# Optimization experiments

Measured on AMD Instinct MI355X. Metric: run time of the kernel, lower is better.

## Reference

```python
import jax, jax.numpy as jnp
import numpy as np
from jax import lax

K = 9  # 3x3 kernel points


def _gather(feat, iy, ix):
    """feat: [B,C,H,W]; iy,ix: [B,K,H,W] int32. Zero padding outside bounds.
    Returns [B,C,K,H,W]."""
    B, C, H, W = feat.shape
    valid = ((iy >= 0) & (iy < H) & (ix >= 0) & (ix < W))
    iyc = jnp.clip(iy, 0, H - 1)
    ixc = jnp.clip(ix, 0, W - 1)
    flat = (iyc * W + ixc).reshape(B, 1, -1)            # [B,1,K*H*W]
    g = jnp.take_along_axis(feat.reshape(B, C, H * W), flat, axis=2)
    g = g.reshape(B, C, K, H, W)
    return g * valid[:, None].astype(feat.dtype)


def _bilinear(feat, ys, xs):
    """feat: [B,C,H,W]; ys,xs: [B,K,H,W] float sampling coords -> [B,C,K,H,W]."""
    y0 = jnp.floor(ys)
    x0 = jnp.floor(xs)
    wy = (ys - y0)[:, None]
    wx = (xs - x0)[:, None]
    y0i = y0.astype(jnp.int32)
    x0i = x0.astype(jnp.int32)
    y1i = y0i + 1
    x1i = x0i + 1
    v00 = _gather(feat, y0i, x0i)
    v01 = _gather(feat, y0i, x1i)
    v10 = _gather(feat, y1i, x0i)
    v11 = _gather(feat, y1i, x1i)
    return (v00 * (1 - wy) * (1 - wx) + v01 * (1 - wy) * wx
            + v10 * wy * (1 - wx) + v11 * wy * wx)


def _deform_layer(x, w_off, b_off, w, b, dilation=1):
    """Modulated deformable 3x3 conv, stride 1, padding=dilation (same size)."""
    B, C, H, W = x.shape
    # offset/mask conv (regular 3x3 conv, same padding)
    om = lax.conv_general_dilated(
        x, w_off, window_strides=(1, 1),
        padding=[(dilation, dilation), (dilation, dilation)],
        rhs_dilation=(dilation, dilation),
        dimension_numbers=('NCHW', 'OIHW', 'NCHW')) + b_off[None, :, None, None]
    off = om[:, :2 * K].reshape(B, K, 2, H, W)   # (dy, dx) per kernel point
    mask = jax.nn.sigmoid(om[:, 2 * K:])         # [B,K,H,W]
    dy = off[:, :, 0]
    dx = off[:, :, 1]
    # base kernel grid offsets (-d, 0, +d)
    ky, kx = jnp.meshgrid(jnp.arange(3), jnp.arange(3), indexing='ij')
    base_y = ((ky.reshape(-1) - 1) * dilation).astype(x.dtype)   # [K]
    base_x = ((kx.reshape(-1) - 1) * dilation).astype(x.dtype)
    gy = jnp.arange(H, dtype=x.dtype)
    gx = jnp.arange(W, dtype=x.dtype)
    ys = gy[None, None, :, None] + base_y[None, :, None, None] + dy  # [B,K,H,W]
    xs = gx[None, None, None, :] + base_x[None, :, None, None] + dx
    sampled = _bilinear(x, ys, xs) * mask[:, None]   # [B,C,K,H,W]
    wk = w.reshape(w.shape[0], w.shape[1], K)        # [O,I,K]
    out = jnp.einsum('bikhw,oik->bohw', sampled, wk) + b[None, :, None, None]
    return out


def setup_inputs() -> dict:
    key = jax.random.key(0)
    ks = jax.random.split(key, 16)
    B, C, H, W = 4, 256, 64, 64
    O = 256
    inp = {'x': jax.random.normal(ks[0], (B, C, H, W), jnp.float32)}
    chans = [(C, C), (C, O), (O, O)]  # layer i==num_layers-2 maps in->out
    for i, (ci, co) in enumerate(chans):
        k = jax.random.split(ks[i + 1], 4)
        # offset conv: 27 = 3*K channels (18 offsets + 9 masks); small init
        inp[f'w_off{i}'] = jax.random.normal(k[0], (3 * K, ci, 3, 3), jnp.float32) * 0.01
        inp[f'b_off{i}'] = jnp.zeros((3 * K,), jnp.float32)
        # deform conv weight: kaiming normal, fan_in = ci*K
        std = np.sqrt(2.0 / (ci * K)).astype(np.float32)
        inp[f'w{i}'] = jax.random.normal(k[1], (co, ci, 3, 3), jnp.float32) * std
        inp[f'b{i}'] = jnp.zeros((co,), jnp.float32)
    return inp


def reference(x, w_off0, b_off0, w0, b0, w_off1, b_off1, w1, b1,
              w_off2, b_off2, w2, b2):
    params = [(w_off0, b_off0, w0, b0),
              (w_off1, b_off1, w1, b1),
              (w_off2, b_off2, w2, b2)]
    for (wo, bo, w, b) in params:
        x = jax.nn.relu(_deform_layer(x, wo, bo, w, b, dilation=1))
    return x
```

## Files before the change

kernel.cpp:

```cpp
#include <hip/hip_runtime.h>
#include <math.h>

#define Bn 4
#define Cn 256
#define Hn 64
#define Wn 64
#define On 256
#define HWn 4096
#define Pn 16384
#define Kc 2304

#define LGKM0 0xc07f

typedef _Float16 half8 __attribute__((ext_vector_type(8)));
typedef float floatx4 __attribute__((ext_vector_type(4)));

__global__ void k_transpose_f2h(const float* __restrict__ in, _Float16* __restrict__ out,
                                int R, int Cc) {
  __shared__ float tile[32][33];
  int b = blockIdx.z;
  int c0 = blockIdx.x * 32, r0 = blockIdx.y * 32;
  const float* ib = in + (size_t)b * R * Cc;
  _Float16* ob = out + (size_t)b * R * Cc;
  int tx = threadIdx.x, ty = threadIdx.y;
#pragma unroll
  for (int i = 0; i < 32; i += 8)
    tile[ty + i][tx] = ib[(size_t)(r0 + ty + i) * Cc + (c0 + tx)];
  __syncthreads();
#pragma unroll
  for (int i = 0; i < 32; i += 8)
    ob[(size_t)(c0 + ty + i) * R + (r0 + tx)] = (_Float16)tile[tx][ty + i];
}

__global__ void k_pack_all(const float* __restrict__ w0, const float* __restrict__ w1,
                           const float* __restrict__ w2, const float* __restrict__ wo0,
                           const float* __restrict__ wo1, const float* __restrict__ wo2,
                           _Float16* __restrict__ wtp, _Float16* __restrict__ wbop) {
  int bx = blockIdx.x;
  int ci = threadIdx.x;
  if (bx < 768) {
    int l = bx >> 8;
    int n = bx & 255;
    const float* w = (l == 0) ? w0 : (l == 1) ? w1 : w2;
    _Float16* dst = wtp + (size_t)l * 256 * Kc;
    int g = n >> 4, col = n & 15;
    int cq = ci >> 6;
    int kk = ci & 63;
    int kq = kk >> 5;
    int k32 = kk & 31;
    int quad = k32 >> 3;
    int e = k32 & 7;
    const float* src = w + (size_t)n * 2304 + (size_t)ci * 9;
#pragma unroll
    for (int t = 0; t < 9; ++t) {
      int c = t * 4 + cq;
      size_t d = ((size_t)((c * 16 + g) * 2 + kq)) * 512 + (quad * 16 + col) * 8 + e;
      dst[d] = (_Float16)src[t];
    }
  } else {
    int b2 = bx - 768;
    int l = b2 >> 5;
    int n = b2 & 31;
    const float* w = (l == 0) ? wo0 : (l == 1) ? wo1 : wo2;
    _Float16* dst = wbop + (size_t)l * 36 * 2048;
    int g = n >> 4, col = n & 15;
    int cw = ci >> 6;
    int r = ci & 63;
    int kq = r >> 5;
    int r2 = r & 31;
    int quad = r2 >> 3;
    int e = r2 & 7;
#pragma unroll
    for (int t = 0; t < 9; ++t) {
      int c = t * 4 + cw;
      size_t d = ((size_t)((c * 2 + g) * 2 + kq)) * 512 + (quad * 16 + col) * 8 + e;
      dst[d] = (n < 27) ? (_Float16)w[((size_t)n * 256 + ci) * 9 + t] : (_Float16)0.f;
    }
  }
}

__global__ __launch_bounds__(256, 4) void k_off_mfma(const _Float16* __restrict__ xh,
                                                     const _Float16* __restrict__ wbop,
                                                     const float* __restrict__ boff,
                                                     float* __restrict__ samp) {
  __shared__ __align__(16) _Float16 Ao[2][32][72];
  __shared__ __align__(16) _Float16 Bo[2][2048];
  __shared__ float omS[32][33];

  int p0 = blockIdx.x * 32;
  int tid = threadIdx.x;
  int lane = tid & 63;
  int wave = tid >> 6;
  int mg = wave >> 1;
  int ng = wave & 1;
  int quad = lane >> 4;
  int col = lane & 15;

  int ar = tid >> 3;
  int aci = (tid & 7) * 8;

  int p = p0 + ar;
  int bimg = p >> 12;
  int yx = p & 4095;
  int y = yx >> 6, x = yx & 63;

  half8 zero8;
#pragma unroll
  for (int e = 0; e < 8; ++e) zero8[e] = (_Float16)0.f;

  floatx4 acc = (floatx4){0.f, 0.f, 0.f, 0.f};

  half8 ga, gb;
  int abase = 0;
  bool avalid = false;

  {
    int sy = y - 1, sx = x - 1;
    avalid = (sy >= 0) & (sy < Hn) & (sx >= 0) & (sx < Wn);
    abase = (((bimg * Hn + (avalid ? sy : 0)) * Wn) + (avalid ? sx : 0)) * Cn;
    ga = zero8;
    if (avalid) ga = *(const half8*)(xh + (size_t)abase + aci);
    gb = *(const half8*)(wbop + (size_t)tid * 8);
  }

#pragma unroll
  for (int c = 0; c < 36; ++c) {
    int buf = c & 1;
    *(half8*)&Ao[buf][ar][aci] = ga;
    *(half8*)&Bo[buf][tid * 8] = gb;

    if (c < 35) {
      int cn = c + 1;
      int tn = cn >> 2;
      int cin = (cn & 3) * 64;
      if ((cn & 3) == 0) {
        int sy = y + tn / 3 - 1;
        int sx = x + tn % 3 - 1;
        avalid = (sy >= 0) & (sy < Hn) & (sx >= 0) & (sx < Wn);
        abase = (((bimg * Hn + (avalid ? sy : 0)) * Wn) + (avalid ? sx : 0)) * Cn;
      }
      ga = zero8;
      if (avalid) ga = *(const half8*)(xh + (size_t)abase + cin + aci);
      gb = *(const half8*)(wbop + (size_t)cn * 2048 + tid * 8);
    }

    __builtin_amdgcn_s_waitcnt(LGKM0);
    __builtin_amdgcn_s_barrier();

    half8 af[2], bf[2];
#pragma unroll
    for (int kq = 0; kq < 2; ++kq) {
      af[kq] = *(const half8*)&Ao[buf][mg * 16 + col][kq * 32 + quad * 8];
      bf[kq] = *(const half8*)&Bo[buf][(ng * 2 + kq) * 512 + lane * 8];
    }
#pragma unroll
    for (int kq = 0; kq < 2; ++kq)
      acc = __builtin_amdgcn_mfma_f32_16x16x32_f16(af[kq], bf[kq], acc, 0, 0, 0);
  }

  int n = ng * 16 + col;
  if (n < 27) {
    float bb = boff[n];
#pragma unroll
    for (int r = 0; r < 4; ++r)
      omS[mg * 16 + quad * 4 + r][n] = acc[r] + bb;
  }
  __syncthreads();

  for (int e = tid; e < 288; e += 256) {
    int lp = e / 9;
    int k = e - lp * 9;
    int pp = p0 + lp;
    int bi = pp >> 12;
    int pyx = pp & 4095;
    int py = pyx >> 6, px = pyx & 63;

    float dy = omS[lp][2 * k];
    float dx = omS[lp][2 * k + 1];
    float m = 1.f / (1.f + expf(-omS[lp][18 + k]));

    float ys = (float)(py + k / 3 - 1) + dy;
    float xs = (float)(px + k % 3 - 1) + dx;
    float y0f = floorf(ys), x0f = floorf(xs);
    float wy = ys - y0f, wx = xs - x0f;
    int y0 = (int)y0f, x0 = (int)x0f;
    int y1 = y0 + 1, x1 = x0 + 1;

    bool vy0 = (y0 >= 0) & (y0 < Hn);
    bool vy1 = (y1 >= 0) & (y1 < Hn);
    bool vx0 = (x0 >= 0) & (x0 < Wn);
    bool vx1 = (x1 >= 0) & (x1 < Wn);
    int y0c = min(max(y0, 0), Hn - 1), y1c = min(max(y1, 0), Hn - 1);
    int x0c = min(max(x0, 0), Wn - 1), x1c = min(max(x1, 0), Wn - 1);

    int base = bi * HWn;
    int o00 = (base + y0c * Wn + x0c) * Cn;
    int o01 = (base + y0c * Wn + x1c) * Cn;
    int o10 = (base + y1c * Wn + x0c) * Cn;
    int o11 = (base + y1c * Wn + x1c) * Cn;

    float w00 = (vy0 && vx0) ? m * (1.f - wy) * (1.f - wx) : 0.f;
    float w01 = (vy0 && vx1) ? m * (1.f - wy) * wx : 0.f;
    float w10 = (vy1 && vx0) ? m * wy * (1.f - wx) : 0.f;
    float w11 = (vy1 && vx1) ? m * wy * wx : 0.f;

    float* s = samp + (size_t)(pp * 9 + k) * 8;
    ((int*)s)[0] = o00; ((int*)s)[1] = o01; ((int*)s)[2] = o10; ((int*)s)[3] = o11;
    s[4] = w00; s[5] = w01; s[6] = w10; s[7] = w11;
  }
}

__global__ __launch_bounds__(512, 2) void k_gemm_main(
    const _Float16* __restrict__ xh, const float* __restrict__ samp,
    const _Float16* __restrict__ wtp, const float* __restrict__ bias,
    _Float16* __restrict__ outh, float* __restrict__ outf) {
  __shared__ __align__(16) _Float16 As[2][64][72];
  __shared__ __align__(16) _Float16 Bs[2][16384];

  int p0 = blockIdx.x * 64;
  int tid = threadIdx.x;
  int lane = tid & 63;
  int wave = tid >> 6;
  int quad = lane >> 4;
  int col = lane & 15;
  int mw = wave >> 2;
  int nw = wave & 3;

  int ar = tid >> 3;
  int aci = (tid & 7) * 8;

  const float* smp = samp + (size_t)(p0 + ar) * 72;

  float bj[4];
#pragma unroll
  for (int j = 0; j < 4; ++j) bj[j] = bias[(nw * 4 + j) * 16 + col];

  floatx4 acc[2][4];
#pragma unroll
  for (int i = 0; i < 2; ++i)
#pragma unroll
    for (int j = 0; j < 4; ++j) acc[i][j] = (floatx4){0.f, 0.f, 0.f, 0.f};

  half8 g00, g01, g10, g11;
  half8 bst[4];
  int4 ofsS[2];
  float4 wvS[2];

  ofsS[0] = *(const int4*)(smp);
  wvS[0] = *(const float4*)(smp + 4);
  g00 = *(const half8*)(xh + (size_t)ofsS[0].x + aci);
  g01 = *(const half8*)(xh + (size_t)ofsS[0].y + aci);
  g10 = *(const half8*)(xh + (size_t)ofsS[0].z + aci);
  g11 = *(const half8*)(xh + (size_t)ofsS[0].w + aci);
#pragma unroll
  for (int q = 0; q < 4; ++q)
    bst[q] = *(const half8*)(wtp + (size_t)(q * 512 + tid) * 8);

#pragma unroll
  for (int c = 0; c < 36; ++c) {
    int buf = c & 1;
    int t = c >> 2;
    {
      float4 wv = wvS[t & 1];
      _Float16 h00 = (_Float16)wv.x, h01 = (_Float16)wv.y;
      _Float16 h10 = (_Float16)wv.z, h11 = (_Float16)wv.w;
      half8 r;
#pragma unroll
      for (int e = 0; e < 8; ++e)
        r[e] = g00[e] * h00 + g01[e] * h01 + g10[e] * h10 + g11[e] * h11;
      *(half8*)&As[buf][ar][aci] = r;
    }
#pragma unroll
    for (int q = 0; q < 4; ++q)
      *(half8*)&Bs[buf][(q * 512 + tid) * 8] = bst[q];

    if (c < 35) {
      int cn = c + 1;
      int tn = cn >> 2;
      int cin = (cn & 3) * 64;
      int4 ofs = ofsS[tn & 1];
      int ci = cin + aci;
      g00 = *(const half8*)(xh + (size_t)ofs.x + ci);
      g01 = *(const half8*)(xh + (size_t)ofs.y + ci);
      g10 = *(const half8*)(xh + (size_t)ofs.z + ci);
      g11 = *(const half8*)(xh + (size_t)ofs.w + ci);
      const _Float16* wsrc = wtp + (size_t)cn * 16384;
#pragma unroll
      for (int q = 0; q < 4; ++q)
        bst[q] = *(const half8*)(wsrc + (size_t)(q * 512 + tid) * 8);
    }
    if ((c & 3) == 0 && t + 1 <= 8) {
      int tnl = t + 1;
      ofsS[tnl & 1] = *(const int4*)(smp + tnl * 8);
      wvS[tnl & 1] = *(const float4*)(smp + tnl * 8 + 4);
    }

    __builtin_amdgcn_s_waitcnt(LGKM0);
    __builtin_amdgcn_s_barrier();

    half8 af[2][2];
#pragma unroll
    for (int kq = 0; kq < 2; ++kq)
#pragma unroll
      for (int i = 0; i < 2; ++i)
        af[kq][i] = *(const half8*)&As[buf][mw * 32 + i * 16 + col][kq * 32 + quad * 8];

    half8 bf[2][4];
#pragma unroll
    for (int kq = 0; kq < 2; ++kq)
#pragma unroll
      for (int j = 0; j < 4; ++j)
        bf[kq][j] = *(const half8*)&Bs[buf][((nw * 4 + j) * 2 + kq) * 512 + lane * 8];

#pragma unroll
    for (int kq = 0; kq < 2; ++kq)
#pragma unroll
      for (int i = 0; i < 2; ++i)
#pragma unroll
        for (int j = 0; j < 4; ++j)
          acc[i][j] = __builtin_amdgcn_mfma_f32_16x16x32_f16(
              af[kq][i], bf[kq][j], acc[i][j], 0, 0, 0);
  }

#pragma unroll
  for (int i = 0; i < 2; ++i)
#pragma unroll
    for (int j = 0; j < 4; ++j) {
      int n = (nw * 4 + j) * 16 + col;
      if (outf) {
        int pb = p0 + mw * 32 + i * 16 + quad * 4;
        int bi = pb >> 12;
        int yx = pb & 4095;
        float4 v;
        v.x = fmaxf(acc[i][j][0] + bj[j], 0.f);
        v.y = fmaxf(acc[i][j][1] + bj[j], 0.f);
        v.z = fmaxf(acc[i][j][2] + bj[j], 0.f);
        v.w = fmaxf(acc[i][j][3] + bj[j], 0.f);
        *(float4*)(outf + ((size_t)(bi * On + n)) * HWn + yx) = v;
      } else {
#pragma unroll
        for (int r = 0; r < 4; ++r) {
          int p = p0 + mw * 32 + i * 16 + quad * 4 + r;
          float v = fmaxf(acc[i][j][r] + bj[j], 0.f);
          outh[(size_t)p * On + n] = (_Float16)v;
        }
      }
    }
}

extern "C" void kernel_launch(void* const* d_in, const int* in_sizes, int n_in,
                              void* d_out, int out_size, void* d_ws, size_t ws_size,
                              hipStream_t stream) {
  (void)in_sizes; (void)n_in; (void)out_size; (void)ws_size;
  const float* x = (const float*)d_in[0];

  _Float16* act0h = (_Float16*)d_ws;
  _Float16* act1h = act0h + (size_t)Pn * Cn;
  float* sampb    = (float*)(act1h + (size_t)Pn * Cn);
  _Float16* wbop  = (_Float16*)(sampb + (size_t)Pn * 9 * 8);
  _Float16* wtp   = wbop + (size_t)3 * 36 * 2048;

  dim3 tb(32, 8);
  k_transpose_f2h<<<dim3(HWn / 32, Cn / 32, Bn), tb, 0, stream>>>(x, act0h, Cn, HWn);
  k_pack_all<<<864, 256, 0, stream>>>(
      (const float*)d_in[3], (const float*)d_in[7], (const float*)d_in[11],
      (const float*)d_in[1], (const float*)d_in[5], (const float*)d_in[9],
      wtp, wbop);

  _Float16* cur = act0h;
  _Float16* nxt = act1h;
  for (int l = 0; l < 3; ++l) {
    const float* b_off = (const float*)d_in[2 + l * 4];
    const float* b     = (const float*)d_in[4 + l * 4];

    k_off_mfma<<<Pn / 32, 256, 0, stream>>>(cur, wbop + (size_t)l * 36 * 2048, b_off, sampb);
    k_gemm_main<<<Pn / 64, 512, 0, stream>>>(cur, sampb, wtp + (size_t)l * 256 * Kc, b, nxt,
                                             (l == 2) ? (float*)d_out : nullptr);
    _Float16* tswap = cur; cur = nxt; nxt = tswap;
  }
}
```

Baseline: 240.4 us.

## Fuse offset conv and deformable GEMM into one per-layer kernel with LDS sampling table

Merges the offset/mask MFMA conv and the main deformable GEMM into a single per-layer kernel. The sampling offsets and weights stay in shared memory instead of going through a global buffer, and the offset-conv staging reuses the main GEMM's LDS. The input transpose and weight packing are also combined into one init kernel. This removes launches and global round-trips of the sample table. In exchange the offset conv runs on 64-row tiles with half the threads idle for the B loads, and __launch_bounds__ drops the occupancy hint, so register pressure and occupancy may change.

```diff
diff --git a/kernel.cpp b/kernel.cpp
--- a/kernel.cpp
+++ b/kernel.cpp
@@ -15,42 +15,41 @@
 typedef _Float16 half8 __attribute__((ext_vector_type(8)));
 typedef float floatx4 __attribute__((ext_vector_type(4)));
 
-__global__ void k_transpose_f2h(const float* __restrict__ in, _Float16* __restrict__ out,
-                                int R, int Cc) {
-  __shared__ float tile[32][33];
-  int b = blockIdx.z;
-  int c0 = blockIdx.x * 32, r0 = blockIdx.y * 32;
-  const float* ib = in + (size_t)b * R * Cc;
-  _Float16* ob = out + (size_t)b * R * Cc;
-  int tx = threadIdx.x, ty = threadIdx.y;
-#pragma unroll
-  for (int i = 0; i < 32; i += 8)
-    tile[ty + i][tx] = ib[(size_t)(r0 + ty + i) * Cc + (c0 + tx)];
-  __syncthreads();
-#pragma unroll
-  for (int i = 0; i < 32; i += 8)
-    ob[(size_t)(c0 + ty + i) * R + (r0 + tx)] = (_Float16)tile[tx][ty + i];
-}
-
-__global__ void k_pack_all(const float* __restrict__ w0, const float* __restrict__ w1,
-                           const float* __restrict__ w2, const float* __restrict__ wo0,
-                           const float* __restrict__ wo1, const float* __restrict__ wo2,
-                           _Float16* __restrict__ wtp, _Float16* __restrict__ wbop) {
+__global__ void k_init(const float* __restrict__ x, _Float16* __restrict__ act0,
+                       const float* __restrict__ w0, const float* __restrict__ w1,
+                       const float* __restrict__ w2, const float* __restrict__ wo0,
+                       const float* __restrict__ wo1, const float* __restrict__ wo2,
+                       _Float16* __restrict__ wtp, _Float16* __restrict__ wbop) {
   int bx = blockIdx.x;
-  int ci = threadIdx.x;
-  if (bx < 768) {
-    int l = bx >> 8;
-    int n = bx & 255;
+  int tid = threadIdx.x;
+  if (bx < 4096) {
+    __shared__ float tile[32][33];
+    int cx = bx & 127, cy = (bx >> 7) & 7, b = bx >> 10;
+    int c0 = cx * 32, r0 = cy * 32;
+    int tx = tid & 31, ty = tid >> 5;
+    const float* ib = x + (size_t)b * Cn * HWn;
+    _Float16* ob = act0 + (size_t)b * Cn * HWn;
+#pragma unroll
+    for (int i = 0; i < 32; i += 8)
+      tile[ty + i][tx] = ib[(size_t)(r0 + ty + i) * HWn + (c0 + tx)];
+    __syncthreads();
+#pragma unroll
+    for (int i = 0; i < 32; i += 8)
+      ob[(size_t)(c0 + ty + i) * Cn + (r0 + tx)] = (_Float16)tile[tx][ty + i];
+  } else if (bx < 4864) {
+    int b2 = bx - 4096;
+    int l = b2 >> 8;
+    int n = b2 & 255;
     const float* w = (l == 0) ? w0 : (l == 1) ? w1 : w2;
     _Float16* dst = wtp + (size_t)l * 256 * Kc;
     int g = n >> 4, col = n & 15;
-    int cq = ci >> 6;
-    int kk = ci & 63;
+    int cq = tid >> 6;
+    int kk = tid & 63;
     int kq = kk >> 5;
     int k32 = kk & 31;
     int quad = k32 >> 3;
     int e = k32 & 7;
-    const float* src = w + (size_t)n * 2304 + (size_t)ci * 9;
+    const float* src = w + (size_t)n * 2304 + (size_t)tid * 9;
 #pragma unroll
     for (int t = 0; t < 9; ++t) {
       int c = t * 4 + cq;
@@ -58,14 +57,14 @@
       dst[d] = (_Float16)src[t];
     }
   } else {
-    int b2 = bx - 768;
-    int l = b2 >> 5;
-    int n = b2 & 31;
+    int b3 = bx - 4864;
+    int l = b3 >> 5;
+    int n = b3 & 31;
     const float* w = (l == 0) ? wo0 : (l == 1) ? wo1 : wo2;
     _Float16* dst = wbop + (size_t)l * 36 * 2048;
     int g = n >> 4, col = n & 15;
-    int cw = ci >> 6;
-    int r = ci & 63;
+    int cw = tid >> 6;
+    int r = tid & 63;
     int kq = r >> 5;
     int r2 = r & 31;
     int quad = r2 >> 3;
@@ -74,25 +73,24 @@
     for (int t = 0; t < 9; ++t) {
       int c = t * 4 + cw;
       size_t d = ((size_t)((c * 2 + g) * 2 + kq)) * 512 + (quad * 16 + col) * 8 + e;
-      dst[d] = (n < 27) ? (_Float16)w[((size_t)n * 256 + ci) * 9 + t] : (_Float16)0.f;
+      dst[d] = (n < 27) ? (_Float16)w[((size_t)n * 256 + tid) * 9 + t] : (_Float16)0.f;
     }
   }
 }
 
-__global__ __launch_bounds__(256, 4) void k_off_mfma(const _Float16* __restrict__ xh,
-                                                     const _Float16* __restrict__ wbop,
-                                                     const float* __restrict__ boff,
-                                                     float* __restrict__ samp) {
-  __shared__ __align__(16) _Float16 Ao[2][32][72];
-  __shared__ __align__(16) _Float16 Bo[2][2048];
-  __shared__ float omS[32][33];
-
-  int p0 = blockIdx.x * 32;
+__global__ __launch_bounds__(512) void k_layer(
+    const _Float16* __restrict__ xh,
+    const _Float16* __restrict__ wbop, const float* __restrict__ boff,
+    const _Float16* __restrict__ wtp, const float* __restrict__ bias,
+    _Float16* __restrict__ outh, float* __restrict__ outf) {
+  __shared__ __align__(16) _Float16 As[2][64][72];
+  __shared__ __align__(16) _Float16 Bs[2][16384];
+  __shared__ __align__(16) float sampS[64][9][8];
+
+  int p0 = blockIdx.x * 64;
   int tid = threadIdx.x;
   int lane = tid & 63;
   int wave = tid >> 6;
-  int mg = wave >> 1;
-  int ng = wave & 1;
   int quad = lane >> 4;
   int col = lane & 15;
 
@@ -108,26 +106,36 @@
 #pragma unroll
   for (int e = 0; e < 8; ++e) zero8[e] = (_Float16)0.f;
 
-  floatx4 acc = (floatx4){0.f, 0.f, 0.f, 0.f};
-
-  half8 ga, gb;
+  half8 bst[4];
+#pragma unroll
+  for (int q = 0; q < 4; ++q)
+    bst[q] = *(const half8*)(wtp + (size_t)(q * 512 + tid) * 8);
+
+  _Float16* Bo0 = &Bs[0][0];
+  _Float16* Bo1 = &Bs[0][2048];
+  float* omS = (float*)&Bs[1][0];
+
+  int mi = wave >> 1;
+  int ng = wave & 1;
+
+  floatx4 acc1 = (floatx4){0.f, 0.f, 0.f, 0.f};
+  half8 ga, gb = zero8;
   int abase = 0;
   bool avalid = false;
-
   {
     int sy = y - 1, sx = x - 1;
     avalid = (sy >= 0) & (sy < Hn) & (sx >= 0) & (sx < Wn);
     abase = (((bimg * Hn + (avalid ? sy : 0)) * Wn) + (avalid ? sx : 0)) * Cn;
     ga = zero8;
     if (avalid) ga = *(const half8*)(xh + (size_t)abase + aci);
-    gb = *(const half8*)(wbop + (size_t)tid * 8);
+    if (tid < 256) gb = *(const half8*)(wbop + (size_t)tid * 8);
   }
 
 #pragma unroll
   for (int c = 0; c < 36; ++c) {
     int buf = c & 1;
-    *(half8*)&Ao[buf][ar][aci] = ga;
-    *(half8*)&Bo[buf][tid * 8] = gb;
+    *(half8*)&As[buf][ar][aci] = ga;
+    if (tid < 256) *(half8*)&(buf ? Bo1 : Bo0)[tid * 8] = gb;
 
     if (c < 35) {
       int cn = c + 1;
@@ -141,33 +149,33 @@
       }
       ga = zero8;
       if (avalid) ga = *(const half8*)(xh + (size_t)abase + cin + aci);
-      gb = *(const half8*)(wbop + (size_t)cn * 2048 + tid * 8);
+      if (tid < 256) gb = *(const half8*)(wbop + (size_t)cn * 2048 + tid * 8);
     }
 
     __builtin_amdgcn_s_waitcnt(LGKM0);
     __builtin_amdgcn_s_barrier();
 
-    half8 af[2], bf[2];
+    const _Float16* BoB = buf ? Bo1 : Bo0;
 #pragma unroll
     for (int kq = 0; kq < 2; ++kq) {
-      af[kq] = *(const half8*)&Ao[buf][mg * 16 + col][kq * 32 + quad * 8];
-      bf[kq] = *(const half8*)&Bo[buf][(ng * 2 + kq) * 512 + lane * 8];
-    }
-#pragma unroll
-    for (int kq = 0; kq < 2; ++kq)
-      acc = __builtin_amdgcn_mfma_f32_16x16x32_f16(af[kq], bf[kq], acc, 0, 0, 0);
-  }
-
-  int n = ng * 16 + col;
-  if (n < 27) {
-    float bb = boff[n];
-#pragma unroll
-    for (int r = 0; r < 4; ++r)
-      omS[mg * 16 + quad * 4 + r][n] = acc[r] + bb;
+      half8 af = *(const half8*)&As[buf][mi * 16 + col][kq * 32 + quad * 8];
+      half8 bf = *(const half8*)&BoB[(ng * 2 + kq) * 512 + lane * 8];
+      acc1 = __builtin_amdgcn_mfma_f32_16x16x32_f16(af, bf, acc1, 0, 0, 0);
+    }
+  }
+
+  {
+    int n1 = ng * 16 + col;
+    if (n1 < 27) {
+      float bb = boff[n1];
+#pragma unroll
+      for (int r = 0; r < 4; ++r)
+        omS[(mi * 16 + quad * 4 + r) * 33 + n1] = acc1[r] + bb;
+    }
   }
   __syncthreads();
 
-  for (int e = tid; e < 288; e += 256) {
+  for (int e = tid; e < 576; e += 512) {
     int lp = e / 9;
     int k = e - lp * 9;
     int pp = p0 + lp;
@@ -175,9 +183,9 @@
     int pyx = pp & 4095;
     int py = pyx >> 6, px = pyx & 63;
 
-    float dy = omS[lp][2 * k];
-    float dx = omS[lp][2 * k + 1];
-    float m = 1.f / (1.f + expf(-omS[lp][18 + k]));
+    float dy = omS[lp * 33 + 2 * k];
+    float dx = omS[lp * 33 + 2 * k + 1];
+    float m = 1.f / (1.f + expf(-omS[lp * 33 + 18 + k]));
 
     float ys = (float)(py + k / 3 - 1) + dy;
     float xs = (float)(px + k % 3 - 1) + dx;
@@ -194,43 +202,21 @@
     int x0c = min(max(x0, 0), Wn - 1), x1c = min(max(x1, 0), Wn - 1);
 
     int base = bi * HWn;
-    int o00 = (base + y0c * Wn + x0c) * Cn;
-    int o01 = (base + y0c * Wn + x1c) * Cn;
-    int o10 = (base + y1c * Wn + x0c) * Cn;
-    int o11 = (base + y1c * Wn + x1c) * Cn;
-
-    float w00 = (vy0 && vx0) ? m * (1.f - wy) * (1.f - wx) : 0.f;
-    float w01 = (vy0 && vx1) ? m * (1.f - wy) * wx : 0.f;
-    float w10 = (vy1 && vx0) ? m * wy * (1.f - wx) : 0.f;
-    float w11 = (vy1 && vx1) ? m * wy * wx : 0.f;
-
-    float* s = samp + (size_t)(pp * 9 + k) * 8;
-    ((int*)s)[0] = o00; ((int*)s)[1] = o01; ((int*)s)[2] = o10; ((int*)s)[3] = o11;
-    s[4] = w00; s[5] = w01; s[6] = w10; s[7] = w11;
-  }
-}
-
-__global__ __launch_bounds__(512, 2) void k_gemm_main(
-    const _Float16* __restrict__ xh, const float* __restrict__ samp,
-    const _Float16* __restrict__ wtp, const float* __restrict__ bias,
-    _Float16* __restrict__ outh, float* __restrict__ outf) {
-  __shared__ __align__(16) _Float16 As[2][64][72];
-  __shared__ __align__(16) _Float16 Bs[2][16384];
-
-  int p0 = blockIdx.x * 64;
-  int tid = threadIdx.x;
-  int lane = tid & 63;
-  int wave = tid >> 6;
-  int quad = lane >> 4;
-  int col = lane & 15;
+    float* s = &sampS[lp][k][0];
+    ((int*)s)[0] = (base + y0c * Wn + x0c) * Cn;
+    ((int*)s)[1] = (base + y0c * Wn + x1c) * Cn;
+    ((int*)s)[2] = (base + y1c * Wn + x0c) * Cn;
+    ((int*)s)[3] = (base + y1c * Wn + x1c) * Cn;
+    s[4] = (vy0 && vx0) ? m * (1.f - wy) * (1.f - wx) : 0.f;
+    s[5] = (vy0 && vx1) ? m * (1.f - wy) * wx : 0.f;
+    s[6] = (vy1 && vx0) ? m * wy * (1.f - wx) : 0.f;
+    s[7] = (vy1 && vx1) ? m * wy * wx : 0.f;
+  }
+  __syncthreads();
+
   int mw = wave >> 2;
   int nw = wave & 3;
 
-  int ar = tid >> 3;
-  int aci = (tid & 7) * 8;
-
-  const float* smp = samp + (size_t)(p0 + ar) * 72;
-
   float bj[4];
 #pragma unroll
   for (int j = 0; j < 4; ++j) bj[j] = bias[(nw * 4 + j) * 16 + col];
@@ -242,19 +228,15 @@
     for (int j = 0; j < 4; ++j) acc[i][j] = (floatx4){0.f, 0.f, 0.f, 0.f};
 
   half8 g00, g01, g10, g11;
-  half8 bst[4];
   int4 ofsS[2];
   float4 wvS[2];
 
-  ofsS[0] = *(const int4*)(smp);
-  wvS[0] = *(const float4*)(smp + 4);
+  ofsS[0] = *(const int4*)&sampS[ar][0][0];
+  wvS[0] = *(const float4*)&sampS[ar][0][4];
   g00 = *(const half8*)(xh + (size_t)ofsS[0].x + aci);
   g01 = *(const half8*)(xh + (size_t)ofsS[0].y + aci);
   g10 = *(const half8*)(xh + (size_t)ofsS[0].z + aci);
   g11 = *(const half8*)(xh + (size_t)ofsS[0].w + aci);
-#pragma unroll
-  for (int q = 0; q < 4; ++q)
-    bst[q] = *(const half8*)(wtp + (size_t)(q * 512 + tid) * 8);
 
 #pragma unroll
   for (int c = 0; c < 36; ++c) {
@@ -291,8 +273,8 @@
     }
     if ((c & 3) == 0 && t + 1 <= 8) {
       int tnl = t + 1;
-      ofsS[tnl & 1] = *(const int4*)(smp + tnl * 8);
-      wvS[tnl & 1] = *(const float4*)(smp + tnl * 8 + 4);
+      ofsS[tnl & 1] = *(const int4*)&sampS[ar][tnl][0];
+      wvS[tnl & 1] = *(const float4*)&sampS[ar][tnl][4];
     }
 
     __builtin_amdgcn_s_waitcnt(LGKM0);
@@ -330,19 +312,19 @@
       if (outf) {
         int pb = p0 + mw * 32 + i * 16 + quad * 4;
         int bi = pb >> 12;
-        int yx = pb & 4095;
+        int pyx = pb & 4095;
         float4 v;
         v.x = fmaxf(acc[i][j][0] + bj[j], 0.f);
         v.y = fmaxf(acc[i][j][1] + bj[j], 0.f);
         v.z = fmaxf(acc[i][j][2] + bj[j], 0.f);
         v.w = fmaxf(acc[i][j][3] + bj[j], 0.f);
-        *(float4*)(outf + ((size_t)(bi * On + n)) * HWn + yx) = v;
+        *(float4*)(outf + ((size_t)(bi * On + n)) * HWn + pyx) = v;
       } else {
 #pragma unroll
         for (int r = 0; r < 4; ++r) {
-          int p = p0 + mw * 32 + i * 16 + quad * 4 + r;
+          int pp = p0 + mw * 32 + i * 16 + quad * 4 + r;
           float v = fmaxf(acc[i][j][r] + bj[j], 0.f);
-          outh[(size_t)p * On + n] = (_Float16)v;
+          outh[(size_t)pp * On + n] = (_Float16)v;
         }
       }
     }
@@ -356,13 +338,11 @@
 
   _Float16* act0h = (_Float16*)d_ws;
   _Float16* act1h = act0h + (size_t)Pn * Cn;
-  float* sampb    = (float*)(act1h + (size_t)Pn * Cn);
-  _Float16* wbop  = (_Float16*)(sampb + (size_t)Pn * 9 * 8);
+  _Float16* wbop  = act1h + (size_t)Pn * Cn;
   _Float16* wtp   = wbop + (size_t)3 * 36 * 2048;
 
-  dim3 tb(32, 8);
-  k_transpose_f2h<<<dim3(HWn / 32, Cn / 32, Bn), tb, 0, stream>>>(x, act0h, Cn, HWn);
-  k_pack_all<<<864, 256, 0, stream>>>(
+  k_init<<<4960, 256, 0, stream>>>(
+      x, act0h,
       (const float*)d_in[3], (const float*)d_in[7], (const float*)d_in[11],
       (const float*)d_in[1], (const float*)d_in[5], (const float*)d_in[9],
       wtp, wbop);
@@ -372,10 +352,10 @@
   for (int l = 0; l < 3; ++l) {
     const float* b_off = (const float*)d_in[2 + l * 4];
     const float* b     = (const float*)d_in[4 + l * 4];
-
-    k_off_mfma<<<Pn / 32, 256, 0, stream>>>(cur, wbop + (size_t)l * 36 * 2048, b_off, sampb);
-    k_gemm_main<<<Pn / 64, 512, 0, stream>>>(cur, sampb, wtp + (size_t)l * 256 * Kc, b, nxt,
-                                             (l == 2) ? (float*)d_out : nullptr);
+    k_layer<<<Pn / 64, 512, 0, stream>>>(
+        cur, wbop + (size_t)l * 36 * 2048, b_off,
+        wtp + (size_t)l * 256 * Kc, b, nxt,
+        (l == 2) ? (float*)d_out : nullptr);
     _Float16* tswap = cur; cur = nxt; nxt = tswap;
   }
 }
```

After: 235.3 us. 2.1% less time.
